# Optimization experiments

Measured on AMD Instinct MI355X. Metric: run time of the kernel, lower is better.

## Reference

```python
import jax, jax.numpy as jnp
import numpy as np

N_WIRES = 12
BLOCK_CONFIGS = [(12, 3), (12, 3)]
HAM_OFFSET = 0.0
HAM_COEFF = 1.0
BATCH = 4096


def _sq(psi, w):
    # view statevector (B, 2^n) as (B, left, 2, right) isolating wire w
    B = psi.shape[0]
    n = N_WIRES
    return psi.reshape(B, 1 << w, 2, 1 << (n - 1 - w))


def _rx(psi, theta, w):
    s = _sq(psi, w)
    t = jnp.asarray(theta, jnp.float32).reshape(-1, 1, 1, 1) * 0.5
    out = jnp.cos(t) * s - 1j * jnp.sin(t) * jnp.flip(s, axis=2)
    return out.reshape(psi.shape)


def _ry(psi, theta, w):
    # [[c,-s],[s,c]]: new = cos*psi + sin*sgn*flip(psi), sgn = (-1, +1)
    s = _sq(psi, w)
    t = jnp.asarray(theta, jnp.float32).reshape(-1, 1, 1, 1) * 0.5
    sgn = jnp.array([-1.0, 1.0], jnp.float32).reshape(1, 1, 2, 1)
    out = jnp.cos(t) * s + jnp.sin(t) * sgn * jnp.flip(s, axis=2)
    return out.reshape(psi.shape)


def _rz(psi, theta, w):
    # diag(e^{-i t/2}, e^{+i t/2})
    s = _sq(psi, w)
    t = jnp.asarray(theta, jnp.float32).reshape(-1, 1, 1, 1) * 0.5
    z = jnp.array([-1.0, 1.0], jnp.float32).reshape(1, 1, 2, 1)
    out = s * jnp.exp(1j * (t * z).astype(jnp.complex64))
    return out.reshape(psi.shape)


def _cnot(psi, c, t):
    B = psi.shape[0]
    n = N_WIRES
    lo, hi = (c, t) if c < t else (t, c)
    s = psi.reshape(B, 1 << lo, 2, 1 << (hi - lo - 1), 2, 1 << (n - 1 - hi))
    ctrl_ax = 2 if c == lo else 4
    tgt_ax = 4 if c == lo else 2
    p0 = jax.lax.index_in_dim(s, 0, axis=ctrl_ax, keepdims=True)
    p1 = jnp.flip(jax.lax.index_in_dim(s, 1, axis=ctrl_ax, keepdims=True), axis=tgt_ax)
    out = jnp.concatenate([p0, p1], axis=ctrl_ax)
    return out.reshape(psi.shape)


def setup_inputs() -> dict:
    key = jax.random.key(0)
    k1, k2 = jax.random.split(key)
    total_encode = sum(ne for ne, _ in BLOCK_CONFIGS)
    total_ansatz = sum(ld for _, ld in BLOCK_CONFIGS)
    x = jax.random.normal(k1, (BATCH, total_encode), dtype=jnp.float32)
    ansatz_weights = jax.random.uniform(
        k2, (total_ansatz, 3, N_WIRES), dtype=jnp.float32,
        minval=-np.pi, maxval=np.pi)
    return {"x": x, "ansatz_weights": ansatz_weights}


def reference(x, ansatz_weights):
    B = x.shape[0]
    n = N_WIRES
    psi = jnp.zeros((B, 1 << n), jnp.complex64).at[:, 0].set(1.0)
    param_col = 0
    ansatz_block = 0
    for n_encode, linear_depth in BLOCK_CONFIGS:
        for j in range(n_encode):
            wire = j % n
            if param_col < x.shape[1]:
                psi = _rx(psi, x[:, param_col], wire)
            param_col += 1
        for _ in range(linear_depth):
            w = ansatz_weights[ansatz_block]
            for i in range(n):
                psi = _ry(psi, w[0, i], i)
                psi = _rz(psi, w[1, i], i)
                psi = _ry(psi, w[2, i], i)
            for i in range(n):
                psi = _cnot(psi, i, (i + 1) % n)
            ansatz_block += 1
    # <H> with H = offset + coeff * sum_i Z_i : diagonal = n - 2*popcount(k)
    probs = psi.real ** 2 + psi.imag ** 2
    k = jnp.arange(1 << n)
    pop = ((k[:, None] >> jnp.arange(n)[None, :]) & 1).sum(-1).astype(jnp.float32)
    diag = HAM_OFFSET + HAM_COEFF * (n - 2.0 * pop)
    expval = probs @ diag  # (B,)
    return expval[:, None]
```

## Files before the change

kernel.cpp:

```cpp
#include <hip/hip_runtime.h>
#include <math.h>

#define NTP 256
#define NT 512
#define NS 4096

typedef float f32x2 __attribute__((ext_vector_type(2)));

constexpr int ring_pi_c(int k) {
    int u = k ^ (k >> 1);
    u ^= u >> 2; u ^= u >> 4; u ^= u >> 8;
    int w0 = ((u >> 11) ^ u) & 1;
    return (u & 0x7FF) | (w0 << 11);
}
constexpr int ring_sigma_c(int k) {
    int s = (k ^ (k >> 1)) & 0x3FF;
    int b10 = ((k >> 10) ^ (k >> 11) ^ k) & 1;
    int b11 = ((k >> 11) ^ k) & 1;
    return s | (b10 << 10) | (b11 << 11);
}
constexpr int swz(int k) {
    int e4 = (k >> 4) & 1, e5 = (k >> 5) & 1, e6 = (k >> 6) & 1;
    return k ^ (e4 | (e5 << 1) | (e6 << 2) | ((e4 ^ e6) << 3));
}

__device__ __forceinline__ void ygate(f32x2 cs_, f32x2& a0, f32x2& a1) {
    f32x2 n0, n1;
    asm("v_pk_mul_f32 %0, %3, %4 op_sel:[0,1] op_sel_hi:[1,1] neg_lo:[0,1] neg_hi:[0,1]\n\t"
        "v_pk_fma_f32 %0, %2, %4, %0 op_sel:[0,0,0] op_sel_hi:[1,0,1]\n\t"
        "v_pk_mul_f32 %1, %2, %4 op_sel:[0,1] op_sel_hi:[1,1]\n\t"
        "v_pk_fma_f32 %1, %3, %4, %1 op_sel:[0,0,0] op_sel_hi:[1,0,1]"
        : "=&v"(n0), "=&v"(n1)
        : "v"(a0), "v"(a1), "v"(cs_));
    a0 = n0; a1 = n1;
}

__device__ __forceinline__ void cdiag(f32x2 e, f32x2& a) {
    f32x2 m;
    asm("v_pk_mul_f32 %0, %1, %2 op_sel:[1,1] op_sel_hi:[0,1] neg_lo:[1,0]\n\t"
        "v_pk_fma_f32 %0, %1, %2, %0 op_sel:[0,0,0] op_sel_hi:[1,0,1]"
        : "=&v"(m) : "v"(a), "v"(e));
    a = m;
}

template<int P>
__device__ __forceinline__ void ygate8(f32x2 a[8], float2 cs_) {
    f32x2 v = f32x2{cs_.x, cs_.y};
    #pragma unroll
    for (int r = 0; r < 8; ++r)
        if (!(r & (1 << P)))
            ygate(v, a[r], a[r | (1 << P)]);
}

__device__ __forceinline__ void wave_lds_fence() {
    asm volatile("s_waitcnt lgkmcnt(0)" ::: "memory");
}

__global__ void prep1_kernel(const float* __restrict__ x,
                             const float* __restrict__ wts,
                             float2* __restrict__ ys,
                             float2* __restrict__ cdah,
                             float2* __restrict__ cs,
                             int total)
{
    int idx = blockIdx.x * blockDim.x + threadIdx.x;
    if (idx < total) {
        float th = 0.5f * x[idx];
        float s, c; sincosf(th, &s, &c);
        cs[idx] = make_float2(c, s);
    }
    if (idx < 72) {
        int ab = idx / 12, w = idx % 12;
        float a  = 0.5f * wts[(ab * 3 + 0) * 12 + w];
        float bb = 0.5f * wts[(ab * 3 + 1) * 12 + w];
        float g  = 0.5f * wts[(ab * 3 + 2) * 12 + w];
        float sa, ca, sb, cb, sg, cg;
        sincosf(a,  &sa, &ca);
        sincosf(bb, &sb, &cb);
        sincosf(g,  &sg, &cg);
        float A = cb * (ca * cg - sa * sg);
        float B = sb * (ca * cg + sa * sg);
        float C = cb * (sa * cg + ca * sg);
        float D = sb * (sa * cg - ca * sg);
        float cy = sqrtf(A * A + B * B);
        float sy = sqrtf(C * C + D * D);
        float f00 = atan2f(-B, A);
        float f10 = atan2f(D, C);
        ys[idx]   = make_float2(cy, sy);
        cdah[idx] = make_float2(0.5f * (f10 - f00), -0.5f * (f10 + f00));
    }
}

__global__ void prep2_kernel(const float2* __restrict__ cdah,
                             float2* __restrict__ tabs)
{
    int idx = blockIdx.x * blockDim.x + threadIdx.x;
    if (idx >= 7 * NS) return;
    int tl = idx >> 12, k = idx & (NS - 1);
    int sk = ring_sigma_c(k);
    const float QP = 0.7853981633974483f;
    float ph = 0.f;
    for (int w = 0; w < 12; ++w) {
        float zd = ((k  >> (11 - w)) & 1) ? 1.f : -1.f;
        float zc = ((sk >> (11 - w)) & 1) ? 1.f : -1.f;
        float dcf, ccf;
        if (tl == 3)      { dcf = QP;                       ccf = cdah[2 * 12 + w].x; }
        else if (tl == 4) { dcf = cdah[3 * 12 + w].y - QP;  ccf = 0.f; }
        else {
            int ald = (tl < 3) ? tl : tl - 1;
            dcf = cdah[ald * 12 + w].y;
            ccf = (tl == 0) ? 0.f : cdah[((tl < 3) ? tl - 1 : tl - 2) * 12 + w].x;
        }
        ph += zd * dcf + zc * ccf;
    }
    float s, c; sincosf(ph, &s, &c);
    tabs[idx] = make_float2(c, s);
}

__global__ __launch_bounds__(NT, 1)
void tqhea_kernel(const float2* __restrict__ ys,
                  const float2* __restrict__ cs,
                  const f32x2*  __restrict__ tabs,
                  float* __restrict__ out)
{
    __shared__ f32x2 psi[NS];

    const int b = blockIdx.x;
    const int t = threadIdx.x;

    const int tsw = swz(t);
    const int sQt = swz(ring_pi_c(t << 3));
    const int Pt  = ring_pi_c(t << 3);

    const float2* csb  = cs + b * 24;
    const float2* cs12 = csb + 12;

    {
        float2 rc[12];
        #pragma unroll
        for (int i = 0; i < 12; ++i) rc[i] = csb[i];
        float mlan = 1.f;
        #pragma unroll
        for (int bit = 0; bit < 9; ++bit)
            mlan *= ((t >> bit) & 1) ? rc[11 - bit].y : rc[11 - bit].x;
        int q = __popc(t);
        #pragma unroll
        for (int r = 0; r < 8; ++r) {
            float mr = 1.f;
            #pragma unroll
            for (int p = 0; p < 3; ++p)
                mr *= ((r >> p) & 1) ? rc[2 - p].y : rc[2 - p].x;
            float mag = mr * mlan;
            int pc = (q + __popc(r)) & 3;
            f32x2 v;
            v.x = (pc == 0) ? mag : ((pc == 2) ? -mag : 0.f);
            v.y = (pc == 1) ? -mag : ((pc == 3) ? mag : 0.f);
            psi[(r << 9) | tsw] = v;
        }
    }
    __syncthreads();

    float acc = 0.f;

    #pragma unroll 1
    for (int lay = 0; lay < 7; ++lay) {
        const bool isx = (lay == 3);
        const float2* yrow = isx ? cs12 : ys + ((lay < 3) ? lay : lay - 1) * 12;
        f32x2 a[8], e[8];

        #pragma unroll
        for (int r = 0; r < 8; ++r) e[r] = tabs[lay * NS + (r << 9) + t];
        #pragma unroll
        for (int r = 0; r < 8; ++r) a[r] = psi[(r << 9) | tsw];
        #pragma unroll
        for (int r = 0; r < 8; ++r) cdiag(e[r], a[r]);
        ygate8<2>(a, yrow[0]);
        ygate8<1>(a, yrow[1]);
        ygate8<0>(a, yrow[2]);
        #pragma unroll
        for (int r = 0; r < 8; ++r) psi[(r << 9) | tsw] = a[r];
        __syncthreads();

        int a1[8];
        #pragma unroll
        for (int r = 0; r < 8; ++r)
            a1[r] = swz(((t >> 6) << 9) | (r << 6) | (t & 63));
        #pragma unroll
        for (int r = 0; r < 8; ++r) a[r] = psi[a1[r]];
        ygate8<2>(a, yrow[3]);
        ygate8<1>(a, yrow[4]);
        ygate8<0>(a, yrow[5]);
        #pragma unroll
        for (int r = 0; r < 8; ++r) psi[a1[r]] = a[r];
        wave_lds_fence();

        int a2[8];
        #pragma unroll
        for (int r = 0; r < 8; ++r)
            a2[r] = swz(((t >> 3) << 6) | (r << 3) | (t & 7));
        #pragma unroll
        for (int r = 0; r < 8; ++r) a[r] = psi[a2[r]];
        ygate8<2>(a, yrow[6]);
        ygate8<1>(a, yrow[7]);
        ygate8<0>(a, yrow[8]);
        #pragma unroll
        for (int r = 0; r < 8; ++r) psi[a2[r]] = a[r];
        wave_lds_fence();

        const int base3 = swz(t << 3);
        #pragma unroll
        for (int r = 0; r < 8; ++r) a[r] = psi[base3 ^ r];
        ygate8<2>(a, yrow[9]);
        ygate8<1>(a, yrow[10]);
        ygate8<0>(a, yrow[11]);
        if (lay == 6) {
            #pragma unroll
            for (int r = 0; r < 8; ++r) {
                float d = 12.0f - 2.0f * (float)__popc(Pt ^ ring_pi_c(r));
                acc += (a[r].x * a[r].x + a[r].y * a[r].y) * d;
            }
        } else if (isx) {
            #pragma unroll
            for (int r = 0; r < 8; ++r) psi[base3 ^ r] = a[r];
            __syncthreads();
        } else {
            __syncthreads();
            #pragma unroll
            for (int r = 0; r < 8; ++r) psi[sQt ^ ring_pi_c(r)] = a[r];
            __syncthreads();
        }
    }

    #pragma unroll
    for (int off = 32; off > 0; off >>= 1)
        acc += __shfl_down(acc, off);
    __syncthreads();
    if ((t & 63) == 0) ((float*)psi)[t >> 6] = acc;
    __syncthreads();
    if (t == 0) {
        const float* rb = (const float*)psi;
        out[b] = rb[0] + rb[1] + rb[2] + rb[3] + rb[4] + rb[5] + rb[6] + rb[7];
    }
}

extern "C" void kernel_launch(void* const* d_in, const int* in_sizes, int n_in,
                              void* d_out, int out_size, void* d_ws, size_t ws_size,
                              hipStream_t stream) {
    const float* x   = (const float*)d_in[0];
    const float* wts = (const float*)d_in[1];
    float* out = (float*)d_out;
    int B = in_sizes[0] / 24;
    int total = B * 24;

    char* ws = (char*)d_ws;
    float2* ys   = (float2*)(ws);
    float2* cdah = (float2*)(ws + 576);
    float2* cs   = (float2*)(ws + 1152);
    float2* tabs = (float2*)(ws + 1152 + (size_t)total * 8);

    prep1_kernel<<<dim3((total + NTP - 1) / NTP), dim3(NTP), 0, stream>>>(x, wts, ys, cdah, cs, total);
    prep2_kernel<<<dim3((7 * NS + NTP - 1) / NTP), dim3(NTP), 0, stream>>>(cdah, tabs);
    tqhea_kernel<<<dim3(B), dim3(NT), 0, stream>>>(ys, cs, (const f32x2*)tabs, out);
}
```

Measured before the change: 189.5 us.

## Fuse second-block RX encoding with first ansatz U3 into complex gates, drop a layer

```diff
diff --git a/kernel.cpp b/kernel.cpp
--- a/kernel.cpp
+++ b/kernel.cpp
@@ -35,6 +35,21 @@
     a0 = n0; a1 = n1;
 }
 
+__device__ __forceinline__ void app1p(f32x2 ab, f32x2 cd, f32x2& a0, f32x2& a1) {
+    f32x2 n0, n1;
+    asm("v_pk_mul_f32 %0, %2, %4 op_sel:[0,0] op_sel_hi:[1,0]\n\t"
+        "v_pk_fma_f32 %0, %2, %4, %0 op_sel:[1,1,0] op_sel_hi:[0,1,1] neg_hi:[0,1,0]\n\t"
+        "v_pk_fma_f32 %0, %3, %5, %0 op_sel:[0,0,0] op_sel_hi:[1,0,1] neg_lo:[0,1,0] neg_hi:[0,1,0]\n\t"
+        "v_pk_fma_f32 %0, %3, %5, %0 op_sel:[1,1,0] op_sel_hi:[0,1,1] neg_lo:[0,1,0]\n\t"
+        "v_pk_mul_f32 %1, %3, %4 op_sel:[0,0] op_sel_hi:[1,0]\n\t"
+        "v_pk_fma_f32 %1, %3, %4, %1 op_sel:[1,1,0] op_sel_hi:[0,1,1] neg_lo:[0,1,0]\n\t"
+        "v_pk_fma_f32 %1, %2, %5, %1 op_sel:[0,0,0] op_sel_hi:[1,0,1]\n\t"
+        "v_pk_fma_f32 %1, %2, %5, %1 op_sel:[1,1,0] op_sel_hi:[0,1,1] neg_lo:[0,1,0]"
+        : "=&v"(n0), "=&v"(n1)
+        : "v"(a0), "v"(a1), "v"(ab), "v"(cd));
+    a0 = n0; a1 = n1;
+}
+
 __device__ __forceinline__ void cdiag(f32x2 e, f32x2& a) {
     f32x2 m;
     asm("v_pk_mul_f32 %0, %1, %2 op_sel:[1,1] op_sel_hi:[0,1] neg_lo:[1,0]\n\t"
@@ -51,15 +66,36 @@
         if (!(r & (1 << P)))
             ygate(v, a[r], a[r | (1 << P)]);
 }
+template<int P>
+__device__ __forceinline__ void cgate8(f32x2 a[8], f32x2 gab, f32x2 gcd) {
+    #pragma unroll
+    for (int r = 0; r < 8; ++r)
+        if (!(r & (1 << P)))
+            app1p(gab, gcd, a[r], a[r | (1 << P)]);
+}
 
 __device__ __forceinline__ void wave_lds_fence() {
     asm volatile("s_waitcnt lgkmcnt(0)" ::: "memory");
+}
+
+__device__ __forceinline__ void load_gate3(const float4* __restrict__ U3w,
+                                           const float2* __restrict__ cs12,
+                                           int w, f32x2& ab, f32x2& cd) {
+    float4 g = U3w[w];
+    float2 sc = cs12[w];
+    float c = sc.x, s = sc.y;
+    float A = g.x * c + g.w * s;
+    float B = g.y * c - g.z * s;
+    float C = g.z * c + g.y * s;
+    float D = g.w * c - g.x * s;
+    ab = f32x2{A, B}; cd = f32x2{C, D};
 }
 
 __global__ void prep1_kernel(const float* __restrict__ x,
                              const float* __restrict__ wts,
                              float2* __restrict__ ys,
                              float2* __restrict__ cdah,
+                             float4* __restrict__ U3w,
                              float2* __restrict__ cs,
                              int total)
 {
@@ -82,6 +118,7 @@
         float B = sb * (ca * cg + sa * sg);
         float C = cb * (sa * cg + ca * sg);
         float D = sb * (sa * cg - ca * sg);
+        if (ab == 3) U3w[w] = make_float4(A, B, C, D);
         float cy = sqrtf(A * A + B * B);
         float sy = sqrtf(C * C + D * D);
         float f00 = atan2f(-B, A);
@@ -95,22 +132,20 @@
                              float2* __restrict__ tabs)
 {
     int idx = blockIdx.x * blockDim.x + threadIdx.x;
-    if (idx >= 7 * NS) return;
+    if (idx >= 6 * NS) return;
     int tl = idx >> 12, k = idx & (NS - 1);
     int sk = ring_sigma_c(k);
-    const float QP = 0.7853981633974483f;
     float ph = 0.f;
     for (int w = 0; w < 12; ++w) {
         float zd = ((k  >> (11 - w)) & 1) ? 1.f : -1.f;
         float zc = ((sk >> (11 - w)) & 1) ? 1.f : -1.f;
-        float dcf, ccf;
-        if (tl == 3)      { dcf = QP;                       ccf = cdah[2 * 12 + w].x; }
-        else if (tl == 4) { dcf = cdah[3 * 12 + w].y - QP;  ccf = 0.f; }
-        else {
-            int ald = (tl < 3) ? tl : tl - 1;
-            dcf = cdah[ald * 12 + w].y;
-            ccf = (tl == 0) ? 0.f : cdah[((tl < 3) ? tl - 1 : tl - 2) * 12 + w].x;
-        }
+        float dcf = 0.f, ccf = 0.f;
+        if (tl == 0)      { dcf = cdah[0 * 12 + w].y; }
+        else if (tl == 1) { dcf = cdah[1 * 12 + w].y; ccf = cdah[0 * 12 + w].x; }
+        else if (tl == 2) { dcf = cdah[2 * 12 + w].y; ccf = cdah[1 * 12 + w].x; }
+        else if (tl == 3) { ccf = cdah[2 * 12 + w].x; }
+        else if (tl == 4) { dcf = cdah[4 * 12 + w].y; }
+        else              { dcf = cdah[5 * 12 + w].y; ccf = cdah[4 * 12 + w].x; }
         ph += zd * dcf + zc * ccf;
     }
     float s, c; sincosf(ph, &s, &c);
@@ -121,6 +156,7 @@
 void tqhea_kernel(const float2* __restrict__ ys,
                   const float2* __restrict__ cs,
                   const f32x2*  __restrict__ tabs,
+                  const float4* __restrict__ U3w,
                   float* __restrict__ out)
 {
     __shared__ f32x2 psi[NS];
@@ -158,25 +194,38 @@
             psi[(r << 9) | tsw] = v;
         }
     }
+
+    f32x2 e[8];
+    #pragma unroll
+    for (int r = 0; r < 8; ++r) e[r] = tabs[(r << 9) + t];
     __syncthreads();
 
     float acc = 0.f;
 
     #pragma unroll 1
-    for (int lay = 0; lay < 7; ++lay) {
-        const bool isx = (lay == 3);
-        const float2* yrow = isx ? cs12 : ys + ((lay < 3) ? lay : lay - 1) * 12;
-        f32x2 a[8], e[8];
-
-        #pragma unroll
-        for (int r = 0; r < 8; ++r) e[r] = tabs[lay * NS + (r << 9) + t];
+    for (int lay = 0; lay < 6; ++lay) {
+        const bool full = (lay == 3);
+        const float2* yrow = ys + lay * 12;
+        f32x2 a[8];
+
         #pragma unroll
         for (int r = 0; r < 8; ++r) a[r] = psi[(r << 9) | tsw];
         #pragma unroll
         for (int r = 0; r < 8; ++r) cdiag(e[r], a[r]);
-        ygate8<2>(a, yrow[0]);
-        ygate8<1>(a, yrow[1]);
-        ygate8<0>(a, yrow[2]);
+        if (lay < 5) {
+            #pragma unroll
+            for (int r = 0; r < 8; ++r) e[r] = tabs[(lay + 1) * NS + (r << 9) + t];
+        }
+        if (full) {
+            f32x2 gab, gcd;
+            load_gate3(U3w, cs12, 0, gab, gcd); cgate8<2>(a, gab, gcd);
+            load_gate3(U3w, cs12, 1, gab, gcd); cgate8<1>(a, gab, gcd);
+            load_gate3(U3w, cs12, 2, gab, gcd); cgate8<0>(a, gab, gcd);
+        } else {
+            ygate8<2>(a, yrow[0]);
+            ygate8<1>(a, yrow[1]);
+            ygate8<0>(a, yrow[2]);
+        }
         #pragma unroll
         for (int r = 0; r < 8; ++r) psi[(r << 9) | tsw] = a[r];
         __syncthreads();
@@ -187,9 +236,16 @@
             a1[r] = swz(((t >> 6) << 9) | (r << 6) | (t & 63));
         #pragma unroll
         for (int r = 0; r < 8; ++r) a[r] = psi[a1[r]];
-        ygate8<2>(a, yrow[3]);
-        ygate8<1>(a, yrow[4]);
-        ygate8<0>(a, yrow[5]);
+        if (full) {
+            f32x2 gab, gcd;
+            load_gate3(U3w, cs12, 3, gab, gcd); cgate8<2>(a, gab, gcd);
+            load_gate3(U3w, cs12, 4, gab, gcd); cgate8<1>(a, gab, gcd);
+            load_gate3(U3w, cs12, 5, gab, gcd); cgate8<0>(a, gab, gcd);
+        } else {
+            ygate8<2>(a, yrow[3]);
+            ygate8<1>(a, yrow[4]);
+            ygate8<0>(a, yrow[5]);
+        }
         #pragma unroll
         for (int r = 0; r < 8; ++r) psi[a1[r]] = a[r];
         wave_lds_fence();
@@ -200,9 +256,16 @@
             a2[r] = swz(((t >> 3) << 6) | (r << 3) | (t & 7));
         #pragma unroll
         for (int r = 0; r < 8; ++r) a[r] = psi[a2[r]];
-        ygate8<2>(a, yrow[6]);
-        ygate8<1>(a, yrow[7]);
-        ygate8<0>(a, yrow[8]);
+        if (full) {
+            f32x2 gab, gcd;
+            load_gate3(U3w, cs12, 6, gab, gcd); cgate8<2>(a, gab, gcd);
+            load_gate3(U3w, cs12, 7, gab, gcd); cgate8<1>(a, gab, gcd);
+            load_gate3(U3w, cs12, 8, gab, gcd); cgate8<0>(a, gab, gcd);
+        } else {
+            ygate8<2>(a, yrow[6]);
+            ygate8<1>(a, yrow[7]);
+            ygate8<0>(a, yrow[8]);
+        }
         #pragma unroll
         for (int r = 0; r < 8; ++r) psi[a2[r]] = a[r];
         wave_lds_fence();
@@ -210,19 +273,22 @@
         const int base3 = swz(t << 3);
         #pragma unroll
         for (int r = 0; r < 8; ++r) a[r] = psi[base3 ^ r];
-        ygate8<2>(a, yrow[9]);
-        ygate8<1>(a, yrow[10]);
-        ygate8<0>(a, yrow[11]);
-        if (lay == 6) {
+        if (full) {
+            f32x2 gab, gcd;
+            load_gate3(U3w, cs12, 9,  gab, gcd); cgate8<2>(a, gab, gcd);
+            load_gate3(U3w, cs12, 10, gab, gcd); cgate8<1>(a, gab, gcd);
+            load_gate3(U3w, cs12, 11, gab, gcd); cgate8<0>(a, gab, gcd);
+        } else {
+            ygate8<2>(a, yrow[9]);
+            ygate8<1>(a, yrow[10]);
+            ygate8<0>(a, yrow[11]);
+        }
+        if (lay == 5) {
             #pragma unroll
             for (int r = 0; r < 8; ++r) {
                 float d = 12.0f - 2.0f * (float)__popc(Pt ^ ring_pi_c(r));
                 acc += (a[r].x * a[r].x + a[r].y * a[r].y) * d;
             }
-        } else if (isx) {
-            #pragma unroll
-            for (int r = 0; r < 8; ++r) psi[base3 ^ r] = a[r];
-            __syncthreads();
         } else {
             __syncthreads();
             #pragma unroll
@@ -255,10 +321,11 @@
     char* ws = (char*)d_ws;
     float2* ys   = (float2*)(ws);
     float2* cdah = (float2*)(ws + 576);
-    float2* cs   = (float2*)(ws + 1152);
-    float2* tabs = (float2*)(ws + 1152 + (size_t)total * 8);
-
-    prep1_kernel<<<dim3((total + NTP - 1) / NTP), dim3(NTP), 0, stream>>>(x, wts, ys, cdah, cs, total);
-    prep2_kernel<<<dim3((7 * NS + NTP - 1) / NTP), dim3(NTP), 0, stream>>>(cdah, tabs);
-    tqhea_kernel<<<dim3(B), dim3(NT), 0, stream>>>(ys, cs, (const f32x2*)tabs, out);
-}
+    float4* U3w  = (float4*)(ws + 1152);
+    float2* cs   = (float2*)(ws + 1344);
+    float2* tabs = (float2*)(ws + 1344 + (size_t)total * 8);
+
+    prep1_kernel<<<dim3((total + NTP - 1) / NTP), dim3(NTP), 0, stream>>>(x, wts, ys, cdah, U3w, cs, total);
+    prep2_kernel<<<dim3((6 * NS + NTP - 1) / NTP), dim3(NTP), 0, stream>>>(cdah, tabs);
+    tqhea_kernel<<<dim3(B), dim3(NT), 0, stream>>>(ys, cs, (const f32x2*)tabs, U3w, out);
+}
```

Result: faster. 185.6 us (-2.0%).
